# Optimization experiments

Hardware: AMD Instinct MI355X
Metric: run time of the kernel (lower is better)

## Reference

```python
import jax, jax.numpy as jnp
import numpy as np

NEG_INF = -1e30  # stand-in for -inf that is safe under softmax
HEADS = 16


def slice_diag_idx(t):
    # result[i, j] = matrix[i, i + j] for matrix of shape (..., t, 2t-1)
    rows = jnp.arange(t)
    cols = rows[:, None] + rows[None, :]  # (t, t), values in [0, 2t-2]
    return rows, cols


def setup_inputs() -> dict:
    key = jax.random.key(0)
    ks = jax.random.split(key, 10)
    b, t, e, h = 4, 1024, 1024, HEADS
    s = e // h
    sc = 0.02
    return {
        "x": jax.random.normal(ks[0], (b, t, e), jnp.float32),
        "Wq": jax.random.normal(ks[1], (e, e), jnp.float32) * sc,
        "Wk": jax.random.normal(ks[2], (e, e), jnp.float32) * sc,
        "Wkp": jax.random.normal(ks[3], (e, e), jnp.float32) * sc,
        "Wv": jax.random.normal(ks[4], (e, e), jnp.float32) * sc,
        "Wu": jax.random.normal(ks[5], (e, e), jnp.float32) * sc,
        "bu": jax.random.normal(ks[6], (e,), jnp.float32) * sc,
        "parma": jax.random.normal(ks[7], (1, h, 1, s), jnp.float32),
        "parmb": jax.random.normal(ks[8], (1, h, 1, s), jnp.float32),
        "pos_emb": jax.random.normal(ks[9], (2 * t - 1, e), jnp.float32),
    }


def reference(x, Wq, Wk, Wkp, Wv, Wu, bu, parma, parmb, pos_emb):
    b, t, e = x.shape
    h = HEADS
    s = e // h

    q = (x @ Wq).reshape(b, t, h, s).transpose(0, 2, 1, 3)   # (b,h,t,s)
    k = (x @ Wk).reshape(b, t, h, s).transpose(0, 2, 1, 3)   # (b,h,t,s)
    v = (x @ Wv).reshape(b, t, h, s).transpose(0, 2, 1, 3)   # (b,h,t,s)
    # positions are identical across batch -> compute once, shape (2t-1,h,s)
    kp = (pos_emb @ Wkp).reshape(2 * t - 1, h, s)

    pa = parma[0, :, 0, :]  # (h,s), broadcast over query position i
    pb = parmb[0, :, 0, :]  # (h,s)

    rows, cols = slice_diag_idx(t)

    # content-content
    dot_tt = jnp.einsum('bhis,bhjs->bhij', q, k)                 # (b,h,t,t)
    # content-position, then slice_diag: [i,j] -> [i, i+j]
    dot_tp_full = jnp.einsum('bhis,jhs->bhij', q, kp)            # (b,h,t,2t-1)
    dot_tp = dot_tp_full[:, :, rows[:, None], cols]              # (b,h,t,t)
    # position-content: constant over query index i
    dot_pt = jnp.einsum('hs,bhjs->bhj', pa, k)[:, :, None, :]    # (b,h,1,t)
    # position-position: constant over i before slicing; slice gives c[i+j]
    c_pp = jnp.einsum('hs,jhs->hj', pb, kp)                      # (h,2t-1)
    dot_pp = c_pp[:, cols][None]                                 # (1,h,t,t)

    dot = dot_tt + dot_tp + dot_pt + dot_pp                      # (b,h,t,t)

    # causal mask: strict upper triangle (j > i) -> -inf
    causal = rows[:, None] >= rows[None, :]                      # (t,t)
    dot = jnp.where(causal[None, None], dot, NEG_INF)

    att = jax.nn.softmax(dot, axis=-1)
    out = jnp.einsum('bhij,bhjs->bhis', att, v)                  # (b,h,t,s)
    out = out.transpose(0, 2, 1, 3).reshape(b, t, e)
    return out @ Wu + bu
```

## Files before the change

kernel.cpp:

```cpp
#include <hip/hip_runtime.h>

typedef unsigned short u16;
typedef unsigned int   u32;
using bf16x8 = __attribute__((ext_vector_type(8))) __bf16;
using f32x4  = __attribute__((ext_vector_type(4))) float;
using u16x8  = __attribute__((ext_vector_type(8))) u16;

#define NEG_INF_F (-1e30f)

__device__ __forceinline__ u16 f2bf(float f) {
  u32 u = __float_as_uint(f);
  u32 r = (u + 0x7FFFu + ((u >> 16) & 1u)) >> 16;
  return (u16)r;
}

__device__ __forceinline__ void async_copy16(const void* g, void* lds) {
  __builtin_amdgcn_global_load_lds(
      (const __attribute__((address_space(1))) void*)g,
      (__attribute__((address_space(3))) void*)lds, 16, 0, 0);
}

__global__ __launch_bounds__(256) void cvt_bf16(const float* __restrict__ in,
                                                u16* __restrict__ out, int n4) {
  int i = blockIdx.x * 256 + threadIdx.x;
  if (i >= n4) return;
  float4 v = reinterpret_cast<const float4*>(in)[i];
  u16 o0 = f2bf(v.x), o1 = f2bf(v.y), o2 = f2bf(v.z), o3 = f2bf(v.w);
  ushort4 o = {o0, o1, o2, o3};
  reinterpret_cast<ushort4*>(out)[i] = o;
}

__global__ __launch_bounds__(256) void cvt_w_tr(
    const float* __restrict__ w0, const float* __restrict__ w1,
    const float* __restrict__ w2, const float* __restrict__ w3,
    const float* __restrict__ w4,
    u16* __restrict__ o0, u16* __restrict__ o1, u16* __restrict__ o2,
    u16* __restrict__ o3, u16* __restrict__ o4) {
  __shared__ float tile[64][65];
  const float* src; u16* dst;
  switch (blockIdx.z) {
    case 0: src = w0; dst = o0; break;
    case 1: src = w1; dst = o1; break;
    case 2: src = w2; dst = o2; break;
    case 3: src = w3; dst = o3; break;
    default: src = w4; dst = o4; break;
  }
  const int tid = threadIdx.x;
  const int r0 = blockIdx.y * 64;
  const int c0 = blockIdx.x * 64;
#pragma unroll
  for (int i = 0; i < 16; ++i) {
    int lin = tid + i * 256;
    int r = lin >> 6, c = lin & 63;
    tile[r][c] = src[(size_t)(r0 + r) * 1024 + c0 + c];
  }
  __syncthreads();
#pragma unroll
  for (int i = 0; i < 16; ++i) {
    int lin = tid + i * 256;
    int n = lin >> 6, k = lin & 63;
    dst[(size_t)(c0 + n) * 1024 + r0 + k] = f2bf(tile[k][n]);
  }
}

__global__ __launch_bounds__(512, 2) void gemm_bf16(
    const u16* __restrict__ A, const u16* __restrict__ Bt,
    float* __restrict__ outF, u16* __restrict__ out0, u16* __restrict__ out1,
    const float* __restrict__ bias0, const float* __restrict__ bias1,
    int M, int mode) {
  __shared__ u16 As[128 * 64];
  __shared__ u16 Bs[128 * 64];
  const int tid = threadIdx.x;
  const int w = tid >> 6, l = tid & 63;
  const int lg = l >> 4, lc = l & 15;
  const int wr = w >> 2, wc = w & 3;
  const int row0 = blockIdx.y * 128;
  const int col0 = blockIdx.x * 128;

  f32x4 acc[4][2];
#pragma unroll
  for (int fi = 0; fi < 4; ++fi)
#pragma unroll
    for (int fj = 0; fj < 2; ++fj) acc[fi][fj] = (f32x4){0.f, 0.f, 0.f, 0.f};

  for (int kb = 0; kb < 1024; kb += 64) {
#pragma unroll
    for (int it2 = 0; it2 < 2; ++it2) {
      int seg = w * 2 + it2;
      int r = seg * 8 + (l >> 3);
      int c8 = (l & 7) * 8;
      int gr = row0 + r; if (gr > M - 1) gr = M - 1;
      async_copy16(&A[(size_t)gr * 1024 + kb + c8], &As[seg * 512]);
      async_copy16(&Bt[(size_t)(col0 + r) * 1024 + kb + c8], &Bs[seg * 512]);
    }
    __syncthreads();
#pragma unroll
    for (int ks = 0; ks < 2; ++ks) {
      bf16x8 af[4], bfr[2];
#pragma unroll
      for (int fi = 0; fi < 4; ++fi)
        af[fi] = *reinterpret_cast<const bf16x8*>(
            &As[(wr * 64 + fi * 16 + lc) * 64 + ks * 32 + lg * 8]);
#pragma unroll
      for (int fj = 0; fj < 2; ++fj)
        bfr[fj] = *reinterpret_cast<const bf16x8*>(
            &Bs[(wc * 32 + fj * 16 + lc) * 64 + ks * 32 + lg * 8]);
#pragma unroll
      for (int fi = 0; fi < 4; ++fi)
#pragma unroll
        for (int fj = 0; fj < 2; ++fj)
          acc[fi][fj] = __builtin_amdgcn_mfma_f32_16x16x32_bf16(
              af[fi], bfr[fj], acc[fi][fj], 0, 0, 0);
    }
    __syncthreads();
  }

#pragma unroll
  for (int fi = 0; fi < 4; ++fi)
#pragma unroll
    for (int fj = 0; fj < 2; ++fj)
#pragma unroll
      for (int reg = 0; reg < 4; ++reg) {
        int R = row0 + wr * 64 + fi * 16 + lg * 4 + reg;
        int C = col0 + wc * 32 + fj * 16 + lc;
        float val = acc[fi][fj][reg];
        if (mode == 3) {
          outF[(size_t)R * 1024 + C] = val + bias0[C];
        } else if (mode == 2) {
          if (R < 2047) {
            int hh = C >> 6, ss = C & 63;
            out0[((size_t)hh * 2047 + R) * 64 + ss] = f2bf(val);
          }
        } else {
          int bi = R >> 10, tt = R & 1023, hh = C >> 6, ss = C & 63;
          size_t o = ((size_t)(bi * 16 + hh) << 16) + (size_t)tt * 64 + ss;
          if (mode == 0) {
            out0[o] = f2bf(val + bias0[C]);
            out1[o] = f2bf(val + bias1[C]);
          } else {
            out0[o] = f2bf(val);
          }
        }
      }
}

__global__ __launch_bounds__(256, 2) void attn_mfma(
    const u16* __restrict__ qa_g, const u16* __restrict__ qb_g,
    const u16* __restrict__ k_g, const u16* __restrict__ v_g,
    const u16* __restrict__ kp_g, u16* __restrict__ ctx) {
  __shared__ u16 kP[64 * 72];
  __shared__ u16 vT[64 * 72];
  __shared__ u16 kpl[128 * 72];
  __shared__ float G[4][16 * 80];

  const int tid = threadIdx.x;
  const int w = tid >> 6, l = tid & 63;
  const int lg = l >> 4, lc = l & 15;
  const int bh = blockIdx.x;
  const int h = bh & 15;
  const int i0 = (15 - (int)blockIdx.y) * 64;
  const size_t bhOff = (size_t)bh << 16;
  const size_t hOff = (size_t)h * 2047 * 64;

  bf16x8 qaf[2], qbf[2];
#pragma unroll
  for (int ks = 0; ks < 2; ++ks) {
    size_t o = bhOff + (size_t)(i0 + w * 16 + lc) * 64 + ks * 32 + lg * 8;
    qaf[ks] = *reinterpret_cast<const bf16x8*>(&qa_g[o]);
    qbf[ks] = *reinterpret_cast<const bf16x8*>(&qb_g[o]);
  }

  f32x4 O[4];
  float m_r[4], l_r[4];
#pragma unroll
  for (int fj = 0; fj < 4; ++fj) O[fj] = (f32x4){0.f, 0.f, 0.f, 0.f};
#pragma unroll
  for (int reg = 0; reg < 4; ++reg) { m_r[reg] = NEG_INF_F; l_r[reg] = 0.f; }

  const int nt = i0 >> 6;
  for (int jt = 0; jt <= nt; ++jt) {
    const int j0 = jt * 64;
    const int pbase = i0 + j0;
    __syncthreads();
#pragma unroll
    for (int rep = 0; rep < 2; ++rep) {
      int idx = tid + rep * 256;
      int jj = idx >> 3, c8 = (idx & 7) * 8;
      *reinterpret_cast<u16x8*>(&kP[jj * 72 + c8]) =
          *reinterpret_cast<const u16x8*>(&k_g[bhOff + (size_t)(j0 + jj) * 64 + c8]);
    }
    {
      int j = tid & 63, s0 = (tid >> 6) * 16;
      u16x8 r0 = *reinterpret_cast<const u16x8*>(&v_g[bhOff + (size_t)(j0 + j) * 64 + s0]);
      u16x8 r1 = *reinterpret_cast<const u16x8*>(&v_g[bhOff + (size_t)(j0 + j) * 64 + s0 + 8]);
#pragma unroll
      for (int i2 = 0; i2 < 8; ++i2) vT[(s0 + i2) * 72 + j] = r0[i2];
#pragma unroll
      for (int i2 = 0; i2 < 8; ++i2) vT[(s0 + 8 + i2) * 72 + j] = r1[i2];
    }
#pragma unroll
    for (int rep = 0; rep < 4; ++rep) {
      int idx = tid + rep * 256;
      int d = idx >> 3, c8 = (idx & 7) * 8;
      int p = pbase + d; if (p > 2046) p = 2046;
      *reinterpret_cast<u16x8*>(&kpl[d * 72 + c8]) =
          *reinterpret_cast<const u16x8*>(&kp_g[hOff + (size_t)p * 64 + c8]);
    }
    __syncthreads();

    f32x4 S[4], Gf[5];
#pragma unroll
    for (int fj = 0; fj < 4; ++fj) S[fj] = (f32x4){0.f, 0.f, 0.f, 0.f};
#pragma unroll
    for (int fg = 0; fg < 5; ++fg) Gf[fg] = (f32x4){0.f, 0.f, 0.f, 0.f};
#pragma unroll
    for (int ks = 0; ks < 2; ++ks) {
#pragma unroll
      for (int fj = 0; fj < 4; ++fj) {
        bf16x8 kf = *reinterpret_cast<const bf16x8*>(
            &kP[(fj * 16 + lc) * 72 + ks * 32 + lg * 8]);
        S[fj] = __builtin_amdgcn_mfma_f32_16x16x32_bf16(qaf[ks], kf, S[fj], 0, 0, 0);
      }
#pragma unroll
      for (int fg = 0; fg < 5; ++fg) {
        bf16x8 pf = *reinterpret_cast<const bf16x8*>(
            &kpl[((w + fg) * 16 + lc) * 72 + ks * 32 + lg * 8]);
        Gf[fg] = __builtin_amdgcn_mfma_f32_16x16x32_bf16(qbf[ks], pf, Gf[fg], 0, 0, 0);
      }
    }
    float* Gw = G[w];
#pragma unroll
    for (int fg = 0; fg < 5; ++fg)
#pragma unroll
      for (int reg = 0; reg < 4; ++reg)
        Gw[(lg * 4 + reg) * 80 + fg * 16 + lc] = Gf[fg][reg];
    asm volatile("s_waitcnt lgkmcnt(0)" ::: "memory");
    __builtin_amdgcn_sched_barrier(0);
#pragma unroll
    for (int fj = 0; fj < 4; ++fj)
#pragma unroll
      for (int reg = 0; reg < 4; ++reg) {
        int rf = lg * 4 + reg;
        float sv = S[fj][reg] + Gw[rf * 80 + rf + fj * 16 + lc];
        if (j0 == i0 && (w * 16 + rf) < (fj * 16 + lc)) sv = NEG_INF_F;
        S[fj][reg] = sv;
      }
#pragma unroll
    for (int reg = 0; reg < 4; ++reg) {
      float mx = fmaxf(fmaxf(S[0][reg], S[1][reg]), fmaxf(S[2][reg], S[3][reg]));
      mx = fmaxf(mx, __shfl_xor(mx, 1));
      mx = fmaxf(mx, __shfl_xor(mx, 2));
      mx = fmaxf(mx, __shfl_xor(mx, 4));
      mx = fmaxf(mx, __shfl_xor(mx, 8));
      float mnew = fmaxf(m_r[reg], mx);
      float corr = __expf(m_r[reg] - mnew);
      float rs = 0.f;
#pragma unroll
      for (int fj = 0; fj < 4; ++fj) {
        float p = __expf(S[fj][reg] - mnew);
        S[fj][reg] = p;
        rs += p;
      }
      rs += __shfl_xor(rs, 1); rs += __shfl_xor(rs, 2);
      rs += __shfl_xor(rs, 4); rs += __shfl_xor(rs, 8);
      l_r[reg] = l_r[reg] * corr + rs;
      m_r[reg] = mnew;
#pragma unroll
      for (int fj = 0; fj < 4; ++fj) O[fj][reg] *= corr;
    }
    __syncthreads();
#pragma unroll
    for (int fj = 0; fj < 4; ++fj)
#pragma unroll
      for (int reg = 0; reg < 4; ++reg)
        kP[(w * 16 + lg * 4 + reg) * 72 + fj * 16 + lc] = f2bf(S[fj][reg]);
    asm volatile("s_waitcnt lgkmcnt(0)" ::: "memory");
    __builtin_amdgcn_sched_barrier(0);
#pragma unroll
    for (int ks = 0; ks < 2; ++ks) {
      bf16x8 pa = *reinterpret_cast<const bf16x8*>(
          &kP[(w * 16 + lc) * 72 + ks * 32 + lg * 8]);
#pragma unroll
      for (int fj = 0; fj < 4; ++fj) {
        bf16x8 vb = *reinterpret_cast<const bf16x8*>(
            &vT[(fj * 16 + lc) * 72 + ks * 32 + lg * 8]);
        O[fj] = __builtin_amdgcn_mfma_f32_16x16x32_bf16(pa, vb, O[fj], 0, 0, 0);
      }
    }
  }

  const int b = bh >> 4;
#pragma unroll
  for (int reg = 0; reg < 4; ++reg) {
    float inv = 1.f / l_r[reg];
    int r = w * 16 + lg * 4 + reg;
#pragma unroll
    for (int fj = 0; fj < 4; ++fj)
      ctx[((size_t)b * 1024 + i0 + r) * 1024 + h * 64 + fj * 16 + lc] =
          f2bf(O[fj][reg] * inv);
  }
}

extern "C" void kernel_launch(void* const* d_in, const int* in_sizes, int n_in,
                              void* d_out, int out_size, void* d_ws, size_t ws_size,
                              hipStream_t stream) {
  const float* x       = (const float*)d_in[0];
  const float* Wq      = (const float*)d_in[1];
  const float* Wk      = (const float*)d_in[2];
  const float* Wkp     = (const float*)d_in[3];
  const float* Wv      = (const float*)d_in[4];
  const float* Wu      = (const float*)d_in[5];
  const float* bu      = (const float*)d_in[6];
  const float* parma   = (const float*)d_in[7];
  const float* parmb   = (const float*)d_in[8];
  const float* pos_emb = (const float*)d_in[9];
  float* out = (float*)d_out;

  u16* W = (u16*)d_ws;
  u16* x_bf   = W;
  u16* pos_bf = x_bf + 4194304;
  u16* wqT    = pos_bf + 2096128;
  u16* wkT    = wqT + 1048576;
  u16* wkpT   = wkT + 1048576;
  u16* wvT    = wkpT + 1048576;
  u16* wuT    = wvT + 1048576;
  u16* qa     = wuT + 1048576;
  u16* qb     = qa + 4194304;
  u16* kb     = qb + 4194304;
  u16* vb     = kb + 4194304;
  u16* kp     = vb + 4194304;
  u16* ctx    = kp + 2096128;

  cvt_bf16<<<4096, 256, 0, stream>>>(x, x_bf, 1048576);
  cvt_bf16<<<2047, 256, 0, stream>>>(pos_emb, pos_bf, 524032);
  cvt_w_tr<<<dim3(16, 16, 5), 256, 0, stream>>>(Wq, Wk, Wkp, Wv, Wu,
                                                wqT, wkT, wkpT, wvT, wuT);
  gemm_bf16<<<dim3(8, 32), 512, 0, stream>>>(x_bf, wqT, nullptr, qa, qb,
                                             parma, parmb, 4096, 0);
  gemm_bf16<<<dim3(8, 32), 512, 0, stream>>>(x_bf, wkT, nullptr, kb, nullptr,
                                             nullptr, nullptr, 4096, 1);
  gemm_bf16<<<dim3(8, 32), 512, 0, stream>>>(x_bf, wvT, nullptr, vb, nullptr,
                                             nullptr, nullptr, 4096, 1);
  gemm_bf16<<<dim3(8, 16), 512, 0, stream>>>(pos_bf, wkpT, nullptr, kp, nullptr,
                                             nullptr, nullptr, 2047, 2);
  attn_mfma<<<dim3(64, 16), 256, 0, stream>>>(qa, qb, kb, vb, kp, ctx);
  gemm_bf16<<<dim3(8, 32), 512, 0, stream>>>(ctx, wuT, out, nullptr, nullptr,
                                             bu, nullptr, 4096, 3);
}
```

Before: 308.9 us.

## Fuse QKV/pos projection GEMMs into one launch and enlarge attention query tile

The four projection GEMMs are merged into one grid: the Q, K and V weights sit contiguously so one launch covers all 3072 output columns, and extra blocks handle the positional projection. The attention kernel now uses 512 threads with a 128-row query tile. Each wave gets its own P buffer, which removes a block barrier, and the next K/V/kp tiles are prefetched into registers. G padding changes to 81 to cut LDS bank conflicts. In exchange the larger tile raises LDS use and needs per-wave causal skipping, which leaves some waves idle on diagonal tiles.

```diff
diff --git a/kernel.cpp b/kernel.cpp
--- a/kernel.cpp
+++ b/kernel.cpp
@@ -63,11 +63,99 @@
   }
 }
 
-__global__ __launch_bounds__(512, 2) void gemm_bf16(
+__global__ __launch_bounds__(512, 2) void gemm_qkvp(
+    const u16* __restrict__ x_bf, const u16* __restrict__ pos_bf,
+    const u16* __restrict__ BtQKV, const u16* __restrict__ BtKP,
+    u16* __restrict__ qa, u16* __restrict__ qb, u16* __restrict__ kb,
+    u16* __restrict__ vb, u16* __restrict__ kp,
+    const float* __restrict__ parma, const float* __restrict__ parmb) {
+  const int bx = blockIdx.x, by = blockIdx.y;
+  const bool isKP = bx >= 24;
+  if (isKP && by >= 16) return;
+
+  __shared__ u16 As[128 * 64];
+  __shared__ u16 Bs[128 * 64];
+  const int tid = threadIdx.x;
+  const int w = tid >> 6, l = tid & 63;
+  const int lg = l >> 4, lc = l & 15;
+  const int wr = w >> 2, wc = w & 3;
+  const u16* A  = isKP ? pos_bf : x_bf;
+  const u16* Bt = isKP ? BtKP : BtQKV;
+  const int M = isKP ? 2047 : 4096;
+  const int row0 = by * 128;
+  const int col0 = (isKP ? (bx - 24) : bx) * 128;
+
+  f32x4 acc[4][2];
+#pragma unroll
+  for (int fi = 0; fi < 4; ++fi)
+#pragma unroll
+    for (int fj = 0; fj < 2; ++fj) acc[fi][fj] = (f32x4){0.f, 0.f, 0.f, 0.f};
+
+  for (int kbk = 0; kbk < 1024; kbk += 64) {
+#pragma unroll
+    for (int it2 = 0; it2 < 2; ++it2) {
+      int seg = w * 2 + it2;
+      int r = seg * 8 + (l >> 3);
+      int c8 = (l & 7) * 8;
+      int gr = row0 + r; if (gr > M - 1) gr = M - 1;
+      async_copy16(&A[(size_t)gr * 1024 + kbk + c8], &As[seg * 512]);
+      async_copy16(&Bt[(size_t)(col0 + r) * 1024 + kbk + c8], &Bs[seg * 512]);
+    }
+    __syncthreads();
+#pragma unroll
+    for (int ks = 0; ks < 2; ++ks) {
+      bf16x8 af[4], bfr[2];
+#pragma unroll
+      for (int fi = 0; fi < 4; ++fi)
+        af[fi] = *reinterpret_cast<const bf16x8*>(
+            &As[(wr * 64 + fi * 16 + lc) * 64 + ks * 32 + lg * 8]);
+#pragma unroll
+      for (int fj = 0; fj < 2; ++fj)
+        bfr[fj] = *reinterpret_cast<const bf16x8*>(
+            &Bs[(wc * 32 + fj * 16 + lc) * 64 + ks * 32 + lg * 8]);
+#pragma unroll
+      for (int fi = 0; fi < 4; ++fi)
+#pragma unroll
+        for (int fj = 0; fj < 2; ++fj)
+          acc[fi][fj] = __builtin_amdgcn_mfma_f32_16x16x32_bf16(
+              af[fi], bfr[fj], acc[fi][fj], 0, 0, 0);
+    }
+    __syncthreads();
+  }
+
+#pragma unroll
+  for (int fi = 0; fi < 4; ++fi)
+#pragma unroll
+    for (int fj = 0; fj < 2; ++fj)
+#pragma unroll
+      for (int reg = 0; reg < 4; ++reg) {
+        int R = row0 + wr * 64 + fi * 16 + lg * 4 + reg;
+        int C = col0 + wc * 32 + fj * 16 + lc;
+        float val = acc[fi][fj][reg];
+        if (isKP) {
+          if (R < 2047) {
+            int hh = C >> 6, ss = C & 63;
+            kp[((size_t)hh * 2047 + R) * 64 + ss] = f2bf(val);
+          }
+        } else {
+          int wsel = C >> 10, Cl = C & 1023;
+          int bi = R >> 10, tt = R & 1023, hh = Cl >> 6, ss = Cl & 63;
+          size_t o = ((size_t)(bi * 16 + hh) << 16) + (size_t)tt * 64 + ss;
+          if (wsel == 0) {
+            qa[o] = f2bf(val + parma[Cl]);
+            qb[o] = f2bf(val + parmb[Cl]);
+          } else if (wsel == 1) {
+            kb[o] = f2bf(val);
+          } else {
+            vb[o] = f2bf(val);
+          }
+        }
+      }
+}
+
+__global__ __launch_bounds__(512, 2) void gemm_out(
     const u16* __restrict__ A, const u16* __restrict__ Bt,
-    float* __restrict__ outF, u16* __restrict__ out0, u16* __restrict__ out1,
-    const float* __restrict__ bias0, const float* __restrict__ bias1,
-    int M, int mode) {
+    float* __restrict__ outF, const float* __restrict__ bias) {
   __shared__ u16 As[128 * 64];
   __shared__ u16 Bs[128 * 64];
   const int tid = threadIdx.x;
@@ -83,15 +171,14 @@
 #pragma unroll
     for (int fj = 0; fj < 2; ++fj) acc[fi][fj] = (f32x4){0.f, 0.f, 0.f, 0.f};
 
-  for (int kb = 0; kb < 1024; kb += 64) {
+  for (int kbk = 0; kbk < 1024; kbk += 64) {
 #pragma unroll
     for (int it2 = 0; it2 < 2; ++it2) {
       int seg = w * 2 + it2;
       int r = seg * 8 + (l >> 3);
       int c8 = (l & 7) * 8;
-      int gr = row0 + r; if (gr > M - 1) gr = M - 1;
-      async_copy16(&A[(size_t)gr * 1024 + kb + c8], &As[seg * 512]);
-      async_copy16(&Bt[(size_t)(col0 + r) * 1024 + kb + c8], &Bs[seg * 512]);
+      async_copy16(&A[(size_t)(row0 + r) * 1024 + kbk + c8], &As[seg * 512]);
+      async_copy16(&Bt[(size_t)(col0 + r) * 1024 + kbk + c8], &Bs[seg * 512]);
     }
     __syncthreads();
 #pragma unroll
@@ -123,42 +210,26 @@
       for (int reg = 0; reg < 4; ++reg) {
         int R = row0 + wr * 64 + fi * 16 + lg * 4 + reg;
         int C = col0 + wc * 32 + fj * 16 + lc;
-        float val = acc[fi][fj][reg];
-        if (mode == 3) {
-          outF[(size_t)R * 1024 + C] = val + bias0[C];
-        } else if (mode == 2) {
-          if (R < 2047) {
-            int hh = C >> 6, ss = C & 63;
-            out0[((size_t)hh * 2047 + R) * 64 + ss] = f2bf(val);
-          }
-        } else {
-          int bi = R >> 10, tt = R & 1023, hh = C >> 6, ss = C & 63;
-          size_t o = ((size_t)(bi * 16 + hh) << 16) + (size_t)tt * 64 + ss;
-          if (mode == 0) {
-            out0[o] = f2bf(val + bias0[C]);
-            out1[o] = f2bf(val + bias1[C]);
-          } else {
-            out0[o] = f2bf(val);
-          }
-        }
-      }
-}
-
-__global__ __launch_bounds__(256, 2) void attn_mfma(
+        outF[(size_t)R * 1024 + C] = acc[fi][fj][reg] + bias[C];
+      }
+}
+
+__global__ __launch_bounds__(512, 2) void attn_mfma(
     const u16* __restrict__ qa_g, const u16* __restrict__ qb_g,
     const u16* __restrict__ k_g, const u16* __restrict__ v_g,
     const u16* __restrict__ kp_g, u16* __restrict__ ctx) {
-  __shared__ u16 kP[64 * 72];
+  __shared__ u16 kT[64 * 72];
   __shared__ u16 vT[64 * 72];
-  __shared__ u16 kpl[128 * 72];
-  __shared__ float G[4][16 * 80];
+  __shared__ u16 kpl[192 * 72];
+  __shared__ float G[8][16 * 81];
+  __shared__ u16 P[8][16 * 72];
 
   const int tid = threadIdx.x;
   const int w = tid >> 6, l = tid & 63;
   const int lg = l >> 4, lc = l & 15;
   const int bh = blockIdx.x;
   const int h = bh & 15;
-  const int i0 = (15 - (int)blockIdx.y) * 64;
+  const int i0 = (7 - (int)blockIdx.y) * 128;
   const size_t bhOff = (size_t)bh << 16;
   const size_t hOff = (size_t)h * 2047 * 64;
 
@@ -170,6 +241,21 @@
     qbf[ks] = *reinterpret_cast<const bf16x8*>(&qb_g[o]);
   }
 
+  const int k_j = tid >> 3, k_c8 = (tid & 7) * 8;
+  const int v_j = tid & 63, v_s0 = (tid >> 6) * 8;
+  u16x8 pk, pv, pp[3];
+  {
+    pk = *reinterpret_cast<const u16x8*>(&k_g[bhOff + (size_t)k_j * 64 + k_c8]);
+    pv = *reinterpret_cast<const u16x8*>(&v_g[bhOff + (size_t)v_j * 64 + v_s0]);
+#pragma unroll
+    for (int r = 0; r < 3; ++r) {
+      int idx = tid + r * 512;
+      int d = idx >> 3, c8 = (idx & 7) * 8;
+      int p = i0 + d; if (p > 2046) p = 2046;
+      pp[r] = *reinterpret_cast<const u16x8*>(&kp_g[hOff + (size_t)p * 64 + c8]);
+    }
+  }
+
   f32x4 O[4];
   float m_r[4], l_r[4];
 #pragma unroll
@@ -177,36 +263,35 @@
 #pragma unroll
   for (int reg = 0; reg < 4; ++reg) { m_r[reg] = NEG_INF_F; l_r[reg] = 0.f; }
 
-  const int nt = i0 >> 6;
-  for (int jt = 0; jt <= nt; ++jt) {
+  const int nt = (i0 >> 6) + 2;
+  for (int jt = 0; jt < nt; ++jt) {
     const int j0 = jt * 64;
-    const int pbase = i0 + j0;
-    __syncthreads();
-#pragma unroll
-    for (int rep = 0; rep < 2; ++rep) {
-      int idx = tid + rep * 256;
-      int jj = idx >> 3, c8 = (idx & 7) * 8;
-      *reinterpret_cast<u16x8*>(&kP[jj * 72 + c8]) =
-          *reinterpret_cast<const u16x8*>(&k_g[bhOff + (size_t)(j0 + jj) * 64 + c8]);
-    }
-    {
-      int j = tid & 63, s0 = (tid >> 6) * 16;
-      u16x8 r0 = *reinterpret_cast<const u16x8*>(&v_g[bhOff + (size_t)(j0 + j) * 64 + s0]);
-      u16x8 r1 = *reinterpret_cast<const u16x8*>(&v_g[bhOff + (size_t)(j0 + j) * 64 + s0 + 8]);
-#pragma unroll
-      for (int i2 = 0; i2 < 8; ++i2) vT[(s0 + i2) * 72 + j] = r0[i2];
-#pragma unroll
-      for (int i2 = 0; i2 < 8; ++i2) vT[(s0 + 8 + i2) * 72 + j] = r1[i2];
-    }
-#pragma unroll
-    for (int rep = 0; rep < 4; ++rep) {
-      int idx = tid + rep * 256;
+    __syncthreads();
+    *reinterpret_cast<u16x8*>(&kT[k_j * 72 + k_c8]) = pk;
+#pragma unroll
+    for (int i2 = 0; i2 < 8; ++i2) vT[(v_s0 + i2) * 72 + v_j] = pv[i2];
+#pragma unroll
+    for (int r = 0; r < 3; ++r) {
+      int idx = tid + r * 512;
       int d = idx >> 3, c8 = (idx & 7) * 8;
-      int p = pbase + d; if (p > 2046) p = 2046;
-      *reinterpret_cast<u16x8*>(&kpl[d * 72 + c8]) =
-          *reinterpret_cast<const u16x8*>(&kp_g[hOff + (size_t)p * 64 + c8]);
-    }
-    __syncthreads();
+      *reinterpret_cast<u16x8*>(&kpl[d * 72 + c8]) = pp[r];
+    }
+    __syncthreads();
+    if (jt + 1 < nt) {
+      const int jn = j0 + 64, pbn = i0 + jn;
+      pk = *reinterpret_cast<const u16x8*>(
+          &k_g[bhOff + (size_t)(jn + k_j) * 64 + k_c8]);
+      pv = *reinterpret_cast<const u16x8*>(
+          &v_g[bhOff + (size_t)(jn + v_j) * 64 + v_s0]);
+#pragma unroll
+      for (int r = 0; r < 3; ++r) {
+        int idx = tid + r * 512;
+        int d = idx >> 3, c8 = (idx & 7) * 8;
+        int p = pbn + d; if (p > 2046) p = 2046;
+        pp[r] = *reinterpret_cast<const u16x8*>(&kp_g[hOff + (size_t)p * 64 + c8]);
+      }
+    }
+    if (j0 > i0 + w * 16 + 15) continue;
 
     f32x4 S[4], Gf[5];
 #pragma unroll
@@ -218,7 +303,7 @@
 #pragma unroll
       for (int fj = 0; fj < 4; ++fj) {
         bf16x8 kf = *reinterpret_cast<const bf16x8*>(
-            &kP[(fj * 16 + lc) * 72 + ks * 32 + lg * 8]);
+            &kT[(fj * 16 + lc) * 72 + ks * 32 + lg * 8]);
         S[fj] = __builtin_amdgcn_mfma_f32_16x16x32_bf16(qaf[ks], kf, S[fj], 0, 0, 0);
       }
 #pragma unroll
@@ -233,16 +318,17 @@
     for (int fg = 0; fg < 5; ++fg)
 #pragma unroll
       for (int reg = 0; reg < 4; ++reg)
-        Gw[(lg * 4 + reg) * 80 + fg * 16 + lc] = Gf[fg][reg];
+        Gw[(lg * 4 + reg) * 81 + fg * 16 + lc] = Gf[fg][reg];
     asm volatile("s_waitcnt lgkmcnt(0)" ::: "memory");
     __builtin_amdgcn_sched_barrier(0);
+    const bool needMask = (j0 + 63 > i0 + w * 16);
 #pragma unroll
     for (int fj = 0; fj < 4; ++fj)
 #pragma unroll
       for (int reg = 0; reg < 4; ++reg) {
         int rf = lg * 4 + reg;
-        float sv = S[fj][reg] + Gw[rf * 80 + rf + fj * 16 + lc];
-        if (j0 == i0 && (w * 16 + rf) < (fj * 16 + lc)) sv = NEG_INF_F;
+        float sv = S[fj][reg] + Gw[rf * 81 + rf + fj * 16 + lc];
+        if (needMask && (i0 + w * 16 + rf) < (j0 + fj * 16 + lc)) sv = NEG_INF_F;
         S[fj][reg] = sv;
       }
 #pragma unroll
@@ -268,18 +354,17 @@
 #pragma unroll
       for (int fj = 0; fj < 4; ++fj) O[fj][reg] *= corr;
     }
-    __syncthreads();
+    u16* Pw = P[w];
 #pragma unroll
     for (int fj = 0; fj < 4; ++fj)
 #pragma unroll
       for (int reg = 0; reg < 4; ++reg)
-        kP[(w * 16 + lg * 4 + reg) * 72 + fj * 16 + lc] = f2bf(S[fj][reg]);
+        Pw[(lg * 4 + reg) * 72 + fj * 16 + lc] = f2bf(S[fj][reg]);
     asm volatile("s_waitcnt lgkmcnt(0)" ::: "memory");
     __builtin_amdgcn_sched_barrier(0);
 #pragma unroll
     for (int ks = 0; ks < 2; ++ks) {
-      bf16x8 pa = *reinterpret_cast<const bf16x8*>(
-          &kP[(w * 16 + lc) * 72 + ks * 32 + lg * 8]);
+      bf16x8 pa = *reinterpret_cast<const bf16x8*>(&Pw[lc * 72 + ks * 32 + lg * 8]);
 #pragma unroll
       for (int fj = 0; fj < 4; ++fj) {
         bf16x8 vb = *reinterpret_cast<const bf16x8*>(
@@ -321,9 +406,9 @@
   u16* pos_bf = x_bf + 4194304;
   u16* wqT    = pos_bf + 2096128;
   u16* wkT    = wqT + 1048576;
-  u16* wkpT   = wkT + 1048576;
-  u16* wvT    = wkpT + 1048576;
-  u16* wuT    = wvT + 1048576;
+  u16* wvT    = wkT + 1048576;
+  u16* wkpT   = wvT + 1048576;
+  u16* wuT    = wkpT + 1048576;
   u16* qa     = wuT + 1048576;
   u16* qb     = qa + 4194304;
   u16* kb     = qb + 4194304;
@@ -335,15 +420,8 @@
   cvt_bf16<<<2047, 256, 0, stream>>>(pos_emb, pos_bf, 524032);
   cvt_w_tr<<<dim3(16, 16, 5), 256, 0, stream>>>(Wq, Wk, Wkp, Wv, Wu,
                                                 wqT, wkT, wkpT, wvT, wuT);
-  gemm_bf16<<<dim3(8, 32), 512, 0, stream>>>(x_bf, wqT, nullptr, qa, qb,
-                                             parma, parmb, 4096, 0);
-  gemm_bf16<<<dim3(8, 32), 512, 0, stream>>>(x_bf, wkT, nullptr, kb, nullptr,
-                                             nullptr, nullptr, 4096, 1);
-  gemm_bf16<<<dim3(8, 32), 512, 0, stream>>>(x_bf, wvT, nullptr, vb, nullptr,
-                                             nullptr, nullptr, 4096, 1);
-  gemm_bf16<<<dim3(8, 16), 512, 0, stream>>>(pos_bf, wkpT, nullptr, kp, nullptr,
-                                             nullptr, nullptr, 2047, 2);
-  attn_mfma<<<dim3(64, 16), 256, 0, stream>>>(qa, qb, kb, vb, kp, ctx);
-  gemm_bf16<<<dim3(8, 32), 512, 0, stream>>>(ctx, wuT, out, nullptr, nullptr,
-                                             bu, nullptr, 4096, 3);
-}
+  gemm_qkvp<<<dim3(32, 32), 512, 0, stream>>>(x_bf, pos_bf, wqT, wkpT,
+                                              qa, qb, kb, vb, kp, parma, parmb);
+  attn_mfma<<<dim3(64, 8), 512, 0, stream>>>(qa, qb, kb, vb, kp, ctx);
+  gemm_out<<<dim3(8, 32), 512, 0, stream>>>(ctx, wuT, out, bu);
+}
```

Result: faster. 252.8 us (-18.2%).
